# Performance work log

Hardware: AMD Instinct MI355X
Metric: run time of the kernel (lower is better)

The kernel has to match this reference:

```python
import jax, jax.numpy as jnp
import numpy as np

B, N, DIM = 4, 2048, 1024
H, DH = 16, 64
SCALE = DH ** -0.5


def setup_inputs() -> dict:
    key = jax.random.key(0)
    k1, k2, k3, k4 = jax.random.split(key, 4)
    x = jax.random.normal(k1, (B, N, DIM), dtype=jnp.float32)
    mask = jax.random.randint(k2, (B, N, N), 0, 2, dtype=jnp.int32)
    W_qkv = jax.random.normal(k3, (DIM, 3 * H * DH), dtype=jnp.float32) * (DIM ** -0.5)
    W_out = jax.random.normal(k4, (H * DH, DIM), dtype=jnp.float32) * ((H * DH) ** -0.5)
    b_out = jnp.zeros((DIM,), dtype=jnp.float32)
    return {"x": x, "mask": mask, "W_qkv": W_qkv, "W_out": W_out, "b_out": b_out}


def reference(x, mask, W_qkv, W_out, b_out):
    # QKV projection: [b, n, 3*h*d]
    qkv = x @ W_qkv
    q, k, v = jnp.split(qkv, 3, axis=-1)
    # 'b n (h d) -> b h n d'
    def to_heads(t):
        b, n, _ = t.shape
        return t.reshape(b, n, H, DH).transpose(0, 2, 1, 3)
    q, k, v = to_heads(q), to_heads(k), to_heads(v)
    # scaled dot-product scores: [b, h, n, n]
    scores = jnp.einsum('bhnd,bhmd->bhnm', q, k) * SCALE
    scores = jnp.where(mask[:, None, :, :] == 1, -jnp.inf, scores)
    att = jax.nn.softmax(scores, axis=-1)
    out = jnp.einsum('bhnm,bhmd->bhnd', att, v)
    # 'b h n d -> b n (h d)'
    out = out.transpose(0, 2, 1, 3).reshape(x.shape[0], x.shape[1], H * DH)
    return out @ W_out + b_out
```

## Files before the change

### kernel.cpp

```cpp
#include <hip/hip_runtime.h>
#include <hip/hip_bf16.h>


typedef __attribute__((ext_vector_type(8))) short bf16x8;
typedef __attribute__((ext_vector_type(4))) float f32x4;

__device__ __forceinline__ unsigned short f2bf(float f) {
  unsigned u = __builtin_bit_cast(unsigned, f);
  u += 0x7fffu + ((u >> 16) & 1u);
  return (unsigned short)(u >> 16);
}

__device__ __forceinline__ void gload16(const void* g, void* l) {
  __builtin_amdgcn_global_load_lds(
      (const __attribute__((address_space(1))) unsigned int*)g,
      (__attribute__((address_space(3))) unsigned int*)l, 16, 0, 0);
}

__device__ __forceinline__ bf16x8 ldsw(const short* base, int row, int elem) {
  const char* p = (const char*)base + row * 128 + ((elem * 2) ^ ((row & 7) << 4));
  return *(const bf16x8*)p;
}

__global__ __launch_bounds__(256) void k_prep(
    const float* __restrict__ x, unsigned short* __restrict__ Xb,
    const float* __restrict__ Wqkv, unsigned short* __restrict__ Wq_t,
    const float* __restrict__ Wout, unsigned short* __restrict__ Wo_t,
    const int* __restrict__ mask, unsigned long long* __restrict__ MP) {
  __shared__ float tile[32][33];
  const int bid = blockIdx.x, t = threadIdx.x;
  if (bid < 8192) {
    int i = (bid * 256 + t) * 4;
    float4 v = *reinterpret_cast<const float4*>(x + i);
    ushort4 o;
    o.x = f2bf(v.x); o.y = f2bf(v.y); o.z = f2bf(v.z); o.w = f2bf(v.w);
    *reinterpret_cast<ushort4*>(Xb + i) = o;
  } else if (bid < 12288) {
    const float* in; unsigned short* out; int rows, cols, bx, by;
    if (bid < 11264) { int l = bid - 8192; in = Wqkv; out = Wq_t; rows = 1024; cols = 3072; bx = l % 96; by = l / 96; }
    else             { int l = bid - 11264; in = Wout; out = Wo_t; rows = 1024; cols = 1024; bx = l & 31; by = l >> 5; }
    int tx = t & 31, ty = t >> 5;
    int c0 = bx * 32, r0 = by * 32;
#pragma unroll
    for (int i = 0; i < 32; i += 8)
      tile[ty + i][tx] = in[(size_t)(r0 + ty + i) * cols + (c0 + tx)];
    __syncthreads();
#pragma unroll
    for (int i = 0; i < 32; i += 8)
      out[(size_t)(c0 + ty + i) * rows + (r0 + tx)] = f2bf(tile[tx][ty + i]);
  } else {
    const int row = bid - 12288;
    const int w = t >> 6, lane = t & 63;
    const int* mrow = mask + (size_t)row * 2048;
#pragma unroll
    for (int it = 0; it < 8; ++it) {
      int key = it * 256 + w * 64 + lane;
      unsigned long long bal = __ballot(mrow[key] == 1);
      if (lane == 0) MP[(size_t)row * 32 + it * 4 + w] = bal;
    }
  }
}

template <int EPI>
__global__ __launch_bounds__(256) void k_gemm(
    const unsigned short* __restrict__ A, const unsigned short* __restrict__ Bt,
    unsigned short* __restrict__ Qo, unsigned short* __restrict__ Ko,
    unsigned short* __restrict__ Vo, float* __restrict__ Co,
    const float* __restrict__ bias) {
  __shared__ __align__(16) short Smem[16896];
  short* As = Smem;
  short* Bs = Smem + 8192;
  const int t = threadIdx.x;
  const int bn = blockIdx.x, bm = blockIdx.y;
  const int wid = t >> 6, lane = t & 63, g = lane >> 4, l15 = lane & 15;
  const int wr = wid >> 1, wc = wid & 1;
  f32x4 zero = {0.f, 0.f, 0.f, 0.f};
  f32x4 acc[4][4];
#pragma unroll
  for (int i = 0; i < 4; ++i)
#pragma unroll
    for (int j = 0; j < 4; ++j) acc[i][j] = zero;

  const char* Ab = (const char*)(A + (size_t)bm * 128 * 1024);
  const char* Bb = (const char*)(Bt + (size_t)bn * 128 * 1024);

  for (int k0 = 0; k0 < 2048; k0 += 128) {
#pragma unroll
    for (int q = 0; q < 4; ++q) {
      int idx = t + q * 256, r = idx >> 3, c = idx & 7;
      int sw = (c * 16) ^ ((r & 7) << 4);
      gload16(Ab + (size_t)r * 2048 + k0 + sw, (char*)As + idx * 16);
      gload16(Bb + (size_t)r * 2048 + k0 + sw, (char*)Bs + idx * 16);
    }
    asm volatile("s_waitcnt vmcnt(0)" ::: "memory");
    __syncthreads();
#pragma unroll
    for (int ks = 0; ks < 2; ++ks) {
      bf16x8 a[4], b[4];
#pragma unroll
      for (int mi = 0; mi < 4; ++mi) a[mi] = ldsw(As, wr * 64 + mi * 16 + l15, ks * 32 + g * 8);
#pragma unroll
      for (int ni = 0; ni < 4; ++ni) b[ni] = ldsw(Bs, wc * 64 + ni * 16 + l15, ks * 32 + g * 8);
#pragma unroll
      for (int mi = 0; mi < 4; ++mi)
#pragma unroll
        for (int ni = 0; ni < 4; ++ni)
          acc[mi][ni] = __builtin_amdgcn_mfma_f32_16x16x32_bf16(a[mi], b[ni], acc[mi][ni], 0, 0, 0);
    }
    __syncthreads();
  }

  if (EPI == 1) {
#pragma unroll
    for (int mi = 0; mi < 4; ++mi)
#pragma unroll
      for (int ni = 0; ni < 4; ++ni)
#pragma unroll
        for (int j = 0; j < 4; ++j) {
          int row = bm * 128 + wr * 64 + mi * 16 + g * 4 + j;
          int col = bn * 128 + wc * 64 + ni * 16 + l15;
          Co[(size_t)row * 1024 + col] = acc[mi][ni][j] + bias[col];
        }
    return;
  }

  const int s = bn >> 3;
  const int h0 = (bn & 7) * 2;
  const int bglob = (bm * 128) >> 11;
  const int n0 = (bm * 128) & 2047;

  if (s < 2) {
    const float qs = (s == 0) ? 0.18033688011112042f : 1.0f;
#pragma unroll
    for (int mi = 0; mi < 4; ++mi)
#pragma unroll
      for (int ni = 0; ni < 4; ++ni)
#pragma unroll
        for (int j = 0; j < 4; ++j)
          Smem[(wr * 64 + mi * 16 + g * 4 + j) * 132 + wc * 64 + ni * 16 + l15] =
              (short)f2bf(acc[mi][ni][j] * qs);
    __syncthreads();
    int r = t >> 1, hh = t & 1;
    unsigned short* dst = (s == 0 ? Qo : Ko) +
        (((size_t)(bglob * 16 + h0 + hh)) * 2048 + n0 + r) * 64;
    const short* src = Smem + r * 132 + hh * 64;
#pragma unroll
    for (int k = 0; k < 8; ++k) {
      uint2 a = *reinterpret_cast<const uint2*>(src + k * 8);
      uint2 b2 = *reinterpret_cast<const uint2*>(src + k * 8 + 4);
      uint4 w = {a.x, a.y, b2.x, b2.y};
      *reinterpret_cast<uint4*>(dst + k * 8) = w;
    }
  } else {
#pragma unroll
    for (int mi = 0; mi < 4; ++mi)
#pragma unroll
      for (int ni = 0; ni < 4; ++ni) {
        unsigned x0 = f2bf(acc[mi][ni][0]), x1 = f2bf(acc[mi][ni][1]);
        unsigned x2 = f2bf(acc[mi][ni][2]), x3 = f2bf(acc[mi][ni][3]);
        uint2 pk = {x0 | (x1 << 16), x2 | (x3 << 16)};
        int col = wc * 64 + ni * 16 + l15;
        int row = wr * 64 + mi * 16 + g * 4;
        *reinterpret_cast<uint2*>(Smem + col * 132 + row) = pk;
      }
    __syncthreads();
    int c = t >> 1, seg = t & 1;
    int h = h0 + (c >> 6), d = c & 63;
    unsigned short* dst = Vo + ((size_t)(bglob * 16 + h) * 64 + d) * 2048 + n0 + seg * 64;
    const short* src = Smem + c * 132 + seg * 64;
#pragma unroll
    for (int k = 0; k < 8; ++k) {
      uint2 a = *reinterpret_cast<const uint2*>(src + k * 8);
      uint2 b2 = *reinterpret_cast<const uint2*>(src + k * 8 + 4);
      uint4 w = {a.x, a.y, b2.x, b2.y};
      *reinterpret_cast<uint4*>(dst + k * 8) = w;
    }
  }
}

__global__ __launch_bounds__(512, 8) void k_attn(
    const unsigned short* __restrict__ Q, const unsigned short* __restrict__ K,
    const unsigned short* __restrict__ Vt_g, const unsigned long long* __restrict__ pack,
    unsigned short* __restrict__ O) {
  __shared__ __align__(16) short Ks[2][64 * 64];
  __shared__ __align__(16) short Vt[2][64 * 64];
  __shared__ __align__(16) short Ps[8][16 * 32];
  const int bid0 = blockIdx.x;
  const int bid = (bid0 & 7) * 128 + (bid0 >> 3);
  const int qt = bid & 15, bh = bid >> 4;
  const int b = bh >> 4;
  const int t = threadIdx.x, wid = t >> 6, lane = t & 63, g = lane >> 4, l15 = lane & 15;
  const char* Kb = (const char*)(K + (size_t)bh * (2048 * 64));
  const char* Vb = (const char*)(Vt_g + (size_t)bh * (64 * 2048));
  const unsigned short* Qb = Q + (size_t)bh * (2048 * 64);

  const int sr = t >> 3, sc = t & 7;
  const int sw_src = (sc * 16) ^ ((sr & 7) << 4);
  char* PwB = (char*)&Ps[wid][0];
  const int ps_rd  = (l15 * 64 + g * 16) ^ ((l15 & 7) << 4);
  const int ps_wr0 = (l15 * 64 + g * 8) ^ ((l15 & 7) << 4);

  gload16(Kb + (size_t)sr * 128 + sw_src, (char*)&Ks[0][0] + t * 16);
  gload16(Vb + (size_t)sr * 4096 + sw_src, (char*)&Vt[0][0] + t * 16);
  const int qrow = qt * 128 + wid * 16 + l15;
  bf16x8 qf0 = *reinterpret_cast<const bf16x8*>(Qb + (size_t)qrow * 64 + g * 8);
  bf16x8 qf1 = *reinterpret_cast<const bf16x8*>(Qb + (size_t)qrow * 64 + 32 + g * 8);
  const unsigned long long* mrow = pack + ((size_t)b * 2048 + qrow) * 32;
  asm volatile("s_waitcnt vmcnt(0)" ::: "memory");
  __syncthreads();

  f32x4 zero = {0.f, 0.f, 0.f, 0.f};
  f32x4 oacc[4];
#pragma unroll
  for (int nf = 0; nf < 4; ++nf) oacc[nf] = zero;
  float lp = 0.f;

  int cb = 0;
#pragma unroll 1
  for (int kt = 0; kt < 32; ++kt) {
    const int nb = cb ^ 1;
    unsigned long long mw = mrow[kt];
    if (kt + 1 < 32) {
      gload16(Kb + (size_t)((kt + 1) * 64 + sr) * 128 + sw_src, (char*)&Ks[nb][0] + t * 16);
      gload16(Vb + (size_t)sr * 4096 + (kt + 1) * 128 + sw_src, (char*)&Vt[nb][0] + t * 16);
    }
    unsigned mlo = (unsigned)mw >> (g * 4);
    unsigned mhi = (unsigned)(mw >> 32) >> (g * 4);
#pragma unroll
    for (int kh = 0; kh < 2; ++kh) {
      f32x4 sf[2] = {zero, zero};
      __builtin_amdgcn_s_setprio(1);
#pragma unroll
      for (int ds = 0; ds < 2; ++ds) {
        bf16x8 qk = ds ? qf1 : qf0;
#pragma unroll
        for (int nf2 = 0; nf2 < 2; ++nf2) {
          bf16x8 kk = ldsw(&Ks[cb][0], (kh * 2 + nf2) * 16 + l15, ds * 32 + g * 8);
          sf[nf2] = __builtin_amdgcn_mfma_f32_16x16x32_bf16(kk, qk, sf[nf2], 0, 0, 0);
        }
      }
      __builtin_amdgcn_s_setprio(0);
      unsigned msrc = kh ? mhi : mlo;
#pragma unroll
      for (int nf2 = 0; nf2 < 2; ++nf2) {
        unsigned eu[4];
#pragma unroll
        for (int j = 0; j < 4; ++j) {
          float s = sf[nf2][j];
          if (msrc & (1u << (nf2 * 16 + j))) s = -1e30f;
          float e = __builtin_amdgcn_exp2f(s);
          lp += e;
          eu[j] = __builtin_bit_cast(unsigned, e);
        }
        uint2 pk;
        pk.x = __builtin_amdgcn_perm(eu[1], eu[0], 0x07060302);
        pk.y = __builtin_amdgcn_perm(eu[3], eu[2], 0x07060302);
        *reinterpret_cast<uint2*>(PwB + (nf2 ? (ps_wr0 ^ 32) : ps_wr0)) = pk;
      }
      asm volatile("s_waitcnt lgkmcnt(0)" ::: "memory");
      __builtin_amdgcn_sched_barrier(0);
      bf16x8 ap = *reinterpret_cast<const bf16x8*>(PwB + ps_rd);
      __builtin_amdgcn_s_setprio(1);
#pragma unroll
      for (int nf = 0; nf < 4; ++nf) {
        bf16x8 bv = ldsw(&Vt[cb][0], nf * 16 + l15, kh * 32 + g * 8);
        oacc[nf] = __builtin_amdgcn_mfma_f32_16x16x32_bf16(ap, bv, oacc[nf], 0, 0, 0);
      }
      __builtin_amdgcn_s_setprio(0);
    }
    asm volatile("s_waitcnt vmcnt(0)" ::: "memory");
    __syncthreads();
    cb = nb;
  }

  float l = lp;
  l += __shfl_xor(l, 16);
  l += __shfl_xor(l, 32);
  float invl = 1.0f / l;
  float inv[4];
#pragma unroll
  for (int j = 0; j < 4; ++j) inv[j] = __shfl(invl, g * 4 + j);

  const int h = bh & 15;
#pragma unroll
  for (int nf = 0; nf < 4; ++nf) {
#pragma unroll
    for (int j = 0; j < 4; ++j) {
      int qg = qt * 128 + wid * 16 + g * 4 + j;
      int d = nf * 16 + l15;
      O[((size_t)b * 2048 + qg) * 1024 + h * 64 + d] = f2bf(oacc[nf][j] * inv[j]);
    }
  }
}

extern "C" void kernel_launch(void* const* d_in, const int* in_sizes, int n_in,
                              void* d_out, int out_size, void* d_ws, size_t ws_size,
                              hipStream_t stream) {
  (void)in_sizes; (void)n_in; (void)out_size; (void)ws_size;
  const float* x = (const float*)d_in[0];
  const int* mask = (const int*)d_in[1];
  const float* Wqkv = (const float*)d_in[2];
  const float* Wout = (const float*)d_in[3];
  const float* bout = (const float*)d_in[4];
  float* out = (float*)d_out;

  unsigned short* ws = (unsigned short*)d_ws;
  unsigned short* Xb   = ws;
  unsigned short* Wq_t = Xb + 8388608;
  unsigned short* Wo_t = Wq_t + 3145728;
  unsigned short* Qa   = Wo_t + 1048576;
  unsigned short* Ka   = Qa + 8388608;
  unsigned short* Va   = Ka + 8388608;
  unsigned short* ATT  = Va + 8388608;
  unsigned long long* MP = (unsigned long long*)(ATT + 8388608);

  k_prep<<<20480, 256, 0, stream>>>(x, Xb, Wqkv, Wq_t, Wout, Wo_t, mask, MP);
  k_gemm<0><<<dim3(24, 64), 256, 0, stream>>>(Xb, Wq_t, Qa, Ka, Va, nullptr, nullptr);
  k_attn<<<1024, 512, 0, stream>>>(Qa, Ka, Va, MP, ATT);
  k_gemm<1><<<dim3(8, 64), 256, 0, stream>>>(ATT, Wo_t, nullptr, nullptr, nullptr, out, bout);
}
```

Before: 238.5 us.

## Single-buffer V tile with mid-iteration barrier and unroll K double-buffer by two

The attention loop now keeps only one V tile in shared memory and issues the V load for the current tile at the start of each iteration. It waits on it with vmcnt(1) plus a block barrier after the first half's QK/softmax, while K remains double-buffered. The loop is manually unrolled by two via a macro so buffer indices are compile-time constants. Launch bounds drop from 8 to 6 waves per SIMD. This cuts LDS use and exposes V latency behind the first half's QK work, at the cost of an extra barrier per tile and lower occupancy.

Measured after the change: 248.8 us. +4.3%, slower.

```diff
diff --git a/kernel.cpp b/kernel.cpp
--- a/kernel.cpp
+++ b/kernel.cpp
@@ -178,12 +178,79 @@
   }
 }
 
-__global__ __launch_bounds__(512, 8) void k_attn(
+#define ATTN_TILE(CBUF, KT, IS_LAST)                                          \
+  {                                                                           \
+    unsigned long long mw = mrow[(KT)];                                       \
+    gload16(Vb + (size_t)(KT) * 128 + vboff, (char*)&Vt[0] + t * 16);         \
+    if (!(IS_LAST))                                                           \
+      gload16(Kb + (size_t)((KT) + 1) * 8192 + kboff,                         \
+              (char*)&Ks[(CBUF) ^ 1][0] + t * 16);                            \
+    unsigned mlo = (unsigned)mw >> (g * 4);                                   \
+    unsigned mhi = (unsigned)(mw >> 32) >> (g * 4);                           \
+    _Pragma("unroll")                                                         \
+    for (int kh = 0; kh < 2; ++kh) {                                          \
+      f32x4 sf[2] = {zero, zero};                                             \
+      __builtin_amdgcn_s_setprio(1);                                          \
+      _Pragma("unroll")                                                       \
+      for (int ds = 0; ds < 2; ++ds) {                                        \
+        bf16x8 qk = ds ? qf1 : qf0;                                           \
+        _Pragma("unroll")                                                     \
+        for (int nf2 = 0; nf2 < 2; ++nf2) {                                   \
+          bf16x8 kk = ldsw(&Ks[(CBUF)][0], (kh * 2 + nf2) * 16 + l15,         \
+                           ds * 32 + g * 8);                                  \
+          sf[nf2] =                                                           \
+              __builtin_amdgcn_mfma_f32_16x16x32_bf16(kk, qk, sf[nf2], 0, 0, 0); \
+        }                                                                     \
+      }                                                                       \
+      __builtin_amdgcn_s_setprio(0);                                         \
+      unsigned msrc = kh ? mhi : mlo;                                         \
+      _Pragma("unroll")                                                       \
+      for (int nf2 = 0; nf2 < 2; ++nf2) {                                     \
+        unsigned eu[4];                                                       \
+        _Pragma("unroll")                                                     \
+        for (int j = 0; j < 4; ++j) {                                         \
+          float s = sf[nf2][j];                                               \
+          if (msrc & (1u << (nf2 * 16 + j))) s = -1e30f;                      \
+          float e = __builtin_amdgcn_exp2f(s);                                \
+          lp += e;                                                            \
+          eu[j] = __builtin_bit_cast(unsigned, e);                            \
+        }                                                                     \
+        uint2 pk;                                                             \
+        pk.x = __builtin_amdgcn_perm(eu[1], eu[0], 0x07060302);               \
+        pk.y = __builtin_amdgcn_perm(eu[3], eu[2], 0x07060302);               \
+        *reinterpret_cast<uint2*>(PwB + (nf2 ? (ps_wr0 ^ 32) : ps_wr0)) = pk; \
+      }                                                                       \
+      if (kh == 0) {                                                          \
+        if (!(IS_LAST))                                                       \
+          asm volatile("s_waitcnt vmcnt(1) lgkmcnt(0)" ::: "memory");         \
+        else                                                                  \
+          asm volatile("s_waitcnt vmcnt(0) lgkmcnt(0)" ::: "memory");         \
+        __builtin_amdgcn_s_barrier();                                         \
+        __builtin_amdgcn_sched_barrier(0);                                    \
+      } else {                                                                \
+        asm volatile("s_waitcnt lgkmcnt(0)" ::: "memory");                    \
+        __builtin_amdgcn_sched_barrier(0);                                    \
+      }                                                                       \
+      bf16x8 ap = *reinterpret_cast<const bf16x8*>(PwB + ps_rd);              \
+      __builtin_amdgcn_s_setprio(1);                                          \
+      _Pragma("unroll")                                                       \
+      for (int nf = 0; nf < 4; ++nf) {                                        \
+        bf16x8 bv = ldsw(&Vt[0], nf * 16 + l15, kh * 32 + g * 8);             \
+        oacc[nf] =                                                            \
+            __builtin_amdgcn_mfma_f32_16x16x32_bf16(ap, bv, oacc[nf], 0, 0, 0); \
+      }                                                                       \
+      __builtin_amdgcn_s_setprio(0);                                         \
+    }                                                                         \
+    asm volatile("s_waitcnt vmcnt(0)" ::: "memory");                          \
+    __builtin_amdgcn_s_barrier();                                            \
+  }
+
+__global__ __launch_bounds__(512, 6) void k_attn(
     const unsigned short* __restrict__ Q, const unsigned short* __restrict__ K,
     const unsigned short* __restrict__ Vt_g, const unsigned long long* __restrict__ pack,
     unsigned short* __restrict__ O) {
   __shared__ __align__(16) short Ks[2][64 * 64];
-  __shared__ __align__(16) short Vt[2][64 * 64];
+  __shared__ __align__(16) short Vt[64 * 64];
   __shared__ __align__(16) short Ps[8][16 * 32];
   const int bid0 = blockIdx.x;
   const int bid = (bid0 & 7) * 128 + (bid0 >> 3);
@@ -196,12 +263,13 @@
 
   const int sr = t >> 3, sc = t & 7;
   const int sw_src = (sc * 16) ^ ((sr & 7) << 4);
+  const int kboff = sr * 128 + sw_src;
+  const int vboff = sr * 4096 + sw_src;
   char* PwB = (char*)&Ps[wid][0];
   const int ps_rd  = (l15 * 64 + g * 16) ^ ((l15 & 7) << 4);
   const int ps_wr0 = (l15 * 64 + g * 8) ^ ((l15 & 7) << 4);
 
-  gload16(Kb + (size_t)sr * 128 + sw_src, (char*)&Ks[0][0] + t * 16);
-  gload16(Vb + (size_t)sr * 4096 + sw_src, (char*)&Vt[0][0] + t * 16);
+  gload16(Kb + kboff, (char*)&Ks[0][0] + t * 16);
   const int qrow = qt * 128 + wid * 16 + l15;
   bf16x8 qf0 = *reinterpret_cast<const bf16x8*>(Qb + (size_t)qrow * 64 + g * 8);
   bf16x8 qf1 = *reinterpret_cast<const bf16x8*>(Qb + (size_t)qrow * 64 + 32 + g * 8);
@@ -215,62 +283,11 @@
   for (int nf = 0; nf < 4; ++nf) oacc[nf] = zero;
   float lp = 0.f;
 
-  int cb = 0;
 #pragma unroll 1
-  for (int kt = 0; kt < 32; ++kt) {
-    const int nb = cb ^ 1;
-    unsigned long long mw = mrow[kt];
-    if (kt + 1 < 32) {
-      gload16(Kb + (size_t)((kt + 1) * 64 + sr) * 128 + sw_src, (char*)&Ks[nb][0] + t * 16);
-      gload16(Vb + (size_t)sr * 4096 + (kt + 1) * 128 + sw_src, (char*)&Vt[nb][0] + t * 16);
-    }
-    unsigned mlo = (unsigned)mw >> (g * 4);
-    unsigned mhi = (unsigned)(mw >> 32) >> (g * 4);
-#pragma unroll
-    for (int kh = 0; kh < 2; ++kh) {
-      f32x4 sf[2] = {zero, zero};
-      __builtin_amdgcn_s_setprio(1);
-#pragma unroll
-      for (int ds = 0; ds < 2; ++ds) {
-        bf16x8 qk = ds ? qf1 : qf0;
-#pragma unroll
-        for (int nf2 = 0; nf2 < 2; ++nf2) {
-          bf16x8 kk = ldsw(&Ks[cb][0], (kh * 2 + nf2) * 16 + l15, ds * 32 + g * 8);
-          sf[nf2] = __builtin_amdgcn_mfma_f32_16x16x32_bf16(kk, qk, sf[nf2], 0, 0, 0);
-        }
-      }
-      __builtin_amdgcn_s_setprio(0);
-      unsigned msrc = kh ? mhi : mlo;
-#pragma unroll
-      for (int nf2 = 0; nf2 < 2; ++nf2) {
-        unsigned eu[4];
-#pragma unroll
-        for (int j = 0; j < 4; ++j) {
-          float s = sf[nf2][j];
-          if (msrc & (1u << (nf2 * 16 + j))) s = -1e30f;
-          float e = __builtin_amdgcn_exp2f(s);
-          lp += e;
-          eu[j] = __builtin_bit_cast(unsigned, e);
-        }
-        uint2 pk;
-        pk.x = __builtin_amdgcn_perm(eu[1], eu[0], 0x07060302);
-        pk.y = __builtin_amdgcn_perm(eu[3], eu[2], 0x07060302);
-        *reinterpret_cast<uint2*>(PwB + (nf2 ? (ps_wr0 ^ 32) : ps_wr0)) = pk;
-      }
-      asm volatile("s_waitcnt lgkmcnt(0)" ::: "memory");
-      __builtin_amdgcn_sched_barrier(0);
-      bf16x8 ap = *reinterpret_cast<const bf16x8*>(PwB + ps_rd);
-      __builtin_amdgcn_s_setprio(1);
-#pragma unroll
-      for (int nf = 0; nf < 4; ++nf) {
-        bf16x8 bv = ldsw(&Vt[cb][0], nf * 16 + l15, kh * 32 + g * 8);
-        oacc[nf] = __builtin_amdgcn_mfma_f32_16x16x32_bf16(ap, bv, oacc[nf], 0, 0, 0);
-      }
-      __builtin_amdgcn_s_setprio(0);
-    }
-    asm volatile("s_waitcnt vmcnt(0)" ::: "memory");
-    __syncthreads();
-    cb = nb;
+  for (int it = 0; it < 16; ++it) {
+    const int kt0 = it * 2;
+    ATTN_TILE(0, kt0, 0)
+    ATTN_TILE(1, kt0 + 1, it == 15)
   }
 
   float l = lp;
```
